# Kernel tuning notes

Hardware: AMD Instinct MI355X
Metric: run time of the kernel (lower is better)

Reference implementation:

```python
import jax, jax.numpy as jnp
import numpy as np
from jax.ops import segment_sum, segment_max

N, E, F, H, G, P, C = 50000, 600000, 128, 128, 64, 32, 10
HEADS = 3
BN_EPS = 1e-5
COS_EPS = 1e-8


def setup_inputs() -> dict:
    key = jax.random.key(0)
    ks = jax.random.split(key, 32)
    rn = lambda k, shape, s: jax.random.normal(k, shape, jnp.float32) * s
    inp = {
        "x": jax.random.normal(ks[0], (N, F), jnp.float32),
        "edge_index": jax.random.randint(ks[1], (2, E), 0, N, jnp.int32),
        "batch": jnp.sort(jax.random.randint(ks[2], (N,), 0, G, jnp.int32)),
        # GCNConv
        "W1": rn(ks[3], (F, H), F ** -0.5), "b1": jnp.zeros((H,), jnp.float32),
        # SAGEConv (lin_l on aggregated neighbors, lin_r on root)
        "Wl": rn(ks[4], (H, H), H ** -0.5), "Wr": rn(ks[5], (H, H), H ** -0.5),
        "bs": jnp.zeros((H,), jnp.float32),
        # GATConv, heads=3, concat=False
        "Wg": rn(ks[6], (H, HEADS * H), H ** -0.5),
        "a_src": rn(ks[7], (HEADS, H), H ** -0.5),
        "a_dst": rn(ks[8], (HEADS, H), H ** -0.5),
        "bg": jnp.zeros((H,), jnp.float32),
        # prototype head / classifier / decoder
        "protos": jax.random.normal(ks[9], (P, H), jnp.float32),
        "Wc": rn(ks[10], (H, C), H ** -0.5), "bc": jnp.zeros((C,), jnp.float32),
        "Wd1": rn(ks[11], (H, 2 * H), H ** -0.5), "bd1": jnp.zeros((2 * H,), jnp.float32),
        "Wd2": rn(ks[12], (2 * H, F), (2 * H) ** -0.5), "bd2": jnp.zeros((F,), jnp.float32),
    }
    # BatchNorm (eval mode): gamma, beta, running mean/var for bn1..bn3
    for i in range(3):
        k0, k1, k2 = jax.random.split(ks[13 + i], 3)
        inp[f"g{i+1}"] = 1.0 + rn(k0, (H,), 0.05)
        inp[f"be{i+1}"] = rn(k1, (H,), 0.05)
        inp[f"m{i+1}"] = rn(k2, (H,), 0.1)
        inp[f"v{i+1}"] = jnp.ones((H,), jnp.float32)
    return inp


def _bn(x, g, b, m, v):
    return (x - m) * jax.lax.rsqrt(v + BN_EPS) * g + b


def _forward(x, edge_index, batch,
             W1, b1, g1, be1, m1, v1,
             Wl, Wr, bs, g2, be2, m2, v2,
             Wg, a_src, a_dst, bg, g3, be3, m3, v3,
             protos, Wc, bc, Wd1, bd1, Wd2, bd2):
    src, dst = edge_index[0], edge_index[1]
    ones_e = jnp.ones((src.shape[0],), x.dtype)

    # --- GCNConv: symmetric norm with self-loops ---
    h = x @ W1                                        # [N, H]
    deg = segment_sum(ones_e, dst, num_segments=N) + 1.0
    dinv = jax.lax.rsqrt(deg)
    coef = dinv[src] * dinv[dst]                      # [E]
    h1 = segment_sum(h[src] * coef[:, None], dst, num_segments=N)
    h1 = h1 + h * (dinv * dinv)[:, None] + b1         # self-loop term + bias
    h1 = jax.nn.elu(_bn(h1, g1, be1, m1, v1))         # dropout = identity (eval)

    # --- SAGEConv: mean aggregation (no self-loops) ---
    cnt = segment_sum(ones_e, dst, num_segments=N)
    mean_nb = segment_sum(h1[src], dst, num_segments=N) / jnp.maximum(cnt, 1.0)[:, None]
    h2 = mean_nb @ Wl + h1 @ Wr + bs
    h2 = jax.nn.elu(_bn(h2, g2, be2, m2, v2))

    # --- GATConv: heads=3, concat=False (mean), with self-loops ---
    hg = (h2 @ Wg).reshape(N, HEADS, H)               # [N, 3, H]
    al_src = jnp.einsum('nhf,hf->nh', hg, a_src)      # [N, 3]
    al_dst = jnp.einsum('nhf,hf->nh', hg, a_dst)
    loop = jnp.arange(N, dtype=src.dtype)
    s2 = jnp.concatenate([src, loop])
    d2 = jnp.concatenate([dst, loop])
    e = jax.nn.leaky_relu(al_src[s2] + al_dst[d2], 0.2)   # [E+N, 3]
    emax = segment_max(e, d2, num_segments=N)             # every node has a self-loop
    ex = jnp.exp(e - emax[d2])
    den = segment_sum(ex, d2, num_segments=N)
    alpha = ex / den[d2]                                  # [E+N, 3]
    h3 = segment_sum(hg[s2] * alpha[:, :, None], d2, num_segments=N)
    h3 = h3.mean(axis=1) + bg                             # concat=False -> head mean
    h3 = jax.nn.elu(_bn(h3, g3, be3, m3, v3))

    # --- global mean pool over graphs ---
    gcnt = segment_sum(jnp.ones((N,), x.dtype), batch, num_segments=G)
    pooled = segment_sum(h3, batch, num_segments=G) / jnp.maximum(gcnt, 1.0)[:, None]

    # --- prototype head: cosine sim -> softmax -> mix ---
    xn = pooled / jnp.maximum(jnp.linalg.norm(pooled, axis=-1, keepdims=True), COS_EPS)
    pn = protos / jnp.maximum(jnp.linalg.norm(protos, axis=-1, keepdims=True), COS_EPS)
    sims = xn @ pn.T                                      # [G, P]
    assignments = jax.nn.softmax(sims, axis=-1)
    proto_emb = assignments @ protos                      # [G, H]
    logits = proto_emb @ Wc + bc                          # [G, C]
    reconstructed = jax.nn.relu(pooled @ Wd1 + bd1) @ Wd2 + bd2   # [G, F]
    return logits, proto_emb, assignments, reconstructed


def reference(x, edge_index, batch,
              W1, b1, g1, be1, m1, v1,
              Wl, Wr, bs, g2, be2, m2, v2,
              Wg, a_src, a_dst, bg, g3, be3, m3, v3,
              protos, Wc, bc, Wd1, bd1, Wd2, bd2):
    return _forward(x, edge_index, batch,
                    W1, b1, g1, be1, m1, v1,
                    Wl, Wr, bs, g2, be2, m2, v2,
                    Wg, a_src, a_dst, bg, g3, be3, m3, v3,
                    protos, Wc, bc, Wd1, bd1, Wd2, bd2)
```

## Files before the change

kernel.cpp:

```cpp
#include <hip/hip_runtime.h>
#include <hip/hip_bf16.h>
#include <stdint.h>
#include <stddef.h>

#define N_ 50000
#define E_ 600000
#define F_ 128
#define H_ 128
#define G_ 64
#define P_ 32
#define C_ 10
#define NB_ 49

typedef __hip_bfloat16 bf16;
typedef __attribute__((ext_vector_type(8))) short short8;
typedef __attribute__((ext_vector_type(4))) float float4v;

__device__ __forceinline__ float b2f(bf16 x){ return __bfloat162float(x); }
__device__ __forceinline__ float us2f(unsigned short u){ return __uint_as_float(((unsigned int)u)<<16); }
__device__ __forceinline__ unsigned short f2us(float x){ bf16 h = __float2bfloat16(x); return *(unsigned short*)&h; }
__device__ __forceinline__ float eluf(float x){ return x>0.f ? x : expm1f(x); }
__device__ __forceinline__ float bnf(float x,float m,float v,float g,float b){ return (x-m)*rsqrtf(v+1e-5f)*g+b; }
__device__ __forceinline__ float lrelu(float x){ return x>0.f ? x : 0.2f*x; }
__device__ __forceinline__ float expc(float x){ return __expf(fminf(x, 50.f)); }
__device__ __forceinline__ void atomAddF(float* a, float v){ unsafeAtomicAdd(a, v); }

__global__ __launch_bounds__(256) void k_wprep(const float* __restrict__ W1, const float* __restrict__ Wl,
    const float* __restrict__ Wr, const float* __restrict__ Wg, unsigned short* __restrict__ WT){
  int idx = blockIdx.x*256 + threadIdx.x;
  if(idx >= 6*16384) return;
  int m = idx >> 14, rem = idx & 16383;
  int n = rem >> 7, k = rem & 127;
  float v;
  if(m==0)      v = W1[k*128+n];
  else if(m==1) v = Wl[k*128+n];
  else if(m==2) v = Wr[k*128+n];
  else          v = Wg[k*384 + (m-3)*128 + n];
  WT[idx] = f2us(v);
}

__device__ __forceinline__ void stage_WT(const unsigned short* __restrict__ WTg, unsigned short* lds, int tid){
  #pragma unroll
  for(int i=0;i<8;i++){
    int idx = tid + i*256;
    int n = idx>>4, c = idx&15;
    uint4 v = *(const uint4*)(WTg + (size_t)idx*8);
    int cs = c ^ (n & 15);
    *(uint4*)(lds + n*128 + cs*8) = v;
  }
}
__device__ __forceinline__ short8 read_Bfrag(const unsigned short* lds, int tile, int kc, int lane){
  int n = tile*16 + (lane&15);
  int c = kc*4 + (lane>>4);
  int cs = c ^ (lane & 15);
  return *(const short8*)(lds + n*128 + cs*8);
}
__device__ __forceinline__ void load_Afrag_bf16(const bf16* A, int row, int lane, short8 af[4]){
  const unsigned short* ap = (const unsigned short*)A + (size_t)row*128 + (lane>>4)*8;
  #pragma unroll
  for(int kc=0;kc<4;kc++) af[kc] = *(const short8*)(ap + kc*32);
}
__device__ __forceinline__ void mfma_pass(const unsigned short* lds, const short8 af[4], int lane, float4v acc[8]){
  #pragma unroll
  for(int tile=0;tile<8;tile++){
    #pragma unroll
    for(int kc=0;kc<4;kc++){
      short8 bfv = read_Bfrag(lds, tile, kc, lane);
      acc[tile] = __builtin_amdgcn_mfma_f32_16x16x32_bf16(af[kc], bfv, acc[tile], 0, 0, 0);
    }
  }
}

__global__ __launch_bounds__(256) void k_mm_x(const float* __restrict__ X, const unsigned short* __restrict__ WTg,
                                              bf16* __restrict__ HB){
  __shared__ unsigned short Wlds[128*128];
  const int tid = threadIdx.x, lane = tid&63, w = tid>>6;
  const int row0 = blockIdx.x*64;
  stage_WT(WTg, Wlds, tid);
  int arow = row0 + w*16 + (lane&15);
  int ar = arow < N_ ? arow : N_-1;
  const float* ap = X + (size_t)ar*128 + (lane>>4)*8;
  short8 af[4];
  #pragma unroll
  for(int kc=0;kc<4;kc++){
    float4 a = *(const float4*)(ap + kc*32);
    float4 b = *(const float4*)(ap + kc*32 + 4);
    short8 v;
    v[0]=(short)f2us(a.x); v[1]=(short)f2us(a.y); v[2]=(short)f2us(a.z); v[3]=(short)f2us(a.w);
    v[4]=(short)f2us(b.x); v[5]=(short)f2us(b.y); v[6]=(short)f2us(b.z); v[7]=(short)f2us(b.w);
    af[kc]=v;
  }
  __syncthreads();
  float4v acc[8];
  #pragma unroll
  for(int t=0;t<8;t++){ acc[t][0]=0.f; acc[t][1]=0.f; acc[t][2]=0.f; acc[t][3]=0.f; }
  mfma_pass(Wlds, af, lane, acc);
  const int colb = lane&15, q = lane>>4;
  unsigned short* ob = (unsigned short*)HB;
  #pragma unroll
  for(int r=0;r<4;r++){
    int ro = row0 + w*16 + q*4 + r;
    if(ro < N_){
      #pragma unroll
      for(int tile=0;tile<8;tile++)
        ob[(size_t)ro*128 + tile*16 + colb] = f2us(acc[tile][r]);
    }
  }
}

__global__ __launch_bounds__(256) void k_sage_mm(const bf16* __restrict__ MaB, const bf16* __restrict__ H1B,
    const unsigned short* __restrict__ WlT, const unsigned short* __restrict__ WrT,
    const float* __restrict__ bs, const float* __restrict__ g2, const float* __restrict__ be2,
    const float* __restrict__ m2, const float* __restrict__ v2, bf16* __restrict__ H2B){
  __shared__ unsigned short Wlds[128*128];
  const int tid = threadIdx.x, lane = tid&63, w = tid>>6;
  const int row0 = blockIdx.x*64;
  int arow = row0 + w*16 + (lane&15);
  int ar = arow < N_ ? arow : N_-1;
  float4v acc[8];
  #pragma unroll
  for(int t=0;t<8;t++){ acc[t][0]=0.f; acc[t][1]=0.f; acc[t][2]=0.f; acc[t][3]=0.f; }
  short8 af[4];

  stage_WT(WlT, Wlds, tid);
  load_Afrag_bf16(MaB, ar, lane, af);
  __syncthreads();
  mfma_pass(Wlds, af, lane, acc);
  __syncthreads();
  stage_WT(WrT, Wlds, tid);
  load_Afrag_bf16(H1B, ar, lane, af);
  __syncthreads();
  mfma_pass(Wlds, af, lane, acc);

  const int colb = lane&15, q = lane>>4;
  unsigned short* ob = (unsigned short*)H2B;
  #pragma unroll
  for(int tile=0;tile<8;tile++){
    int col = tile*16 + colb;
    float bsv=bs[col], gv=g2[col], bev=be2[col], mv=m2[col], vv=v2[col];
    #pragma unroll
    for(int r=0;r<4;r++){
      int ro = row0 + w*16 + q*4 + r;
      if(ro < N_){
        float x = acc[tile][r] + bsv;
        ob[(size_t)ro*128 + col] = f2us(eluf(bnf(x, mv, vv, gv, bev)));
      }
    }
  }
}

__global__ __launch_bounds__(256) void k_gat_mm_all(const bf16* __restrict__ H2B, const unsigned short* __restrict__ WgT,
    const float* __restrict__ a_src, const float* __restrict__ a_dst,
    bf16* __restrict__ HG3, float* __restrict__ als3, float* __restrict__ ald3){
  __shared__ unsigned short Wlds[128*128];
  const int tid = threadIdx.x, lane = tid&63, w = tid>>6;
  const int row0 = blockIdx.x*64;
  int arow = row0 + w*16 + (lane&15);
  int ar = arow < N_ ? arow : N_-1;
  short8 af[4];
  load_Afrag_bf16(H2B, ar, lane, af);
  const int colb = lane&15, q = lane>>4;
  unsigned short* ob = (unsigned short*)HG3;
  for(int hh=0; hh<3; hh++){
    if(hh) __syncthreads();
    stage_WT(WgT + hh*16384, Wlds, tid);
    __syncthreads();
    float4v acc[8];
    #pragma unroll
    for(int t=0;t<8;t++){ acc[t][0]=0.f; acc[t][1]=0.f; acc[t][2]=0.f; acc[t][3]=0.f; }
    mfma_pass(Wlds, af, lane, acc);
    float asv[8], adv[8];
    #pragma unroll
    for(int tile=0;tile<8;tile++){
      asv[tile] = a_src[hh*128 + tile*16 + colb];
      adv[tile] = a_dst[hh*128 + tile*16 + colb];
    }
    #pragma unroll
    for(int r=0;r<4;r++){
      int ro = row0 + w*16 + q*4 + r;
      float ps = 0.f, pd = 0.f;
      #pragma unroll
      for(int tile=0;tile<8;tile++){ ps += acc[tile][r]*asv[tile]; pd += acc[tile][r]*adv[tile]; }
      #pragma unroll
      for(int o=8;o>0;o>>=1){ ps += __shfl_down(ps,o,16); pd += __shfl_down(pd,o,16); }
      if(ro < N_){
        #pragma unroll
        for(int tile=0;tile<8;tile++)
          ob[(size_t)ro*384 + hh*128 + tile*16 + colb] = f2us(acc[tile][r]);
        if(colb == 0){ als3[ro*3+hh] = ps; ald3[ro*3+hh] = pd; }
      }
    }
  }
}

__global__ __launch_bounds__(256) void k_count(const int* __restrict__ dst, int* __restrict__ cnt){
  int e = blockIdx.x*256 + threadIdx.x;
  if(e < E_) atomicAdd(&cnt[dst[e]], 1);
}

__global__ __launch_bounds__(1024) void k_scan1(const int* __restrict__ cnt, int* __restrict__ row_ptr,
                                                float* __restrict__ dinv, int* __restrict__ bsum){
  __shared__ int wsum[16];
  const int t = threadIdx.x, lane = t & 63, wid = t >> 6;
  int i = blockIdx.x*1024 + t;
  int v = (i<N_) ? cnt[i] : 0;
  int x = v;
  #pragma unroll
  for(int o=1;o<64;o<<=1){
    int y = __shfl_up(x, o, 64);
    if(lane >= o) x += y;
  }
  if(lane==63) wsum[wid] = x;
  __syncthreads();
  if(wid==0){
    int s = (lane<16) ? wsum[lane] : 0;
    #pragma unroll
    for(int o=1;o<16;o<<=1){
      int y = __shfl_up(s, o, 64);
      if(lane >= o) s += y;
    }
    if(lane<16) wsum[lane] = s;
  }
  __syncthreads();
  int waveoff = (wid>0) ? wsum[wid-1] : 0;
  int incl = waveoff + x;
  if(i<N_){
    row_ptr[i] = incl - v;
    dinv[i] = rsqrtf((float)v + 1.f);
  }
  if(t==1023) bsum[blockIdx.x] = incl;
}

__global__ __launch_bounds__(64) void k_scan2(const int* __restrict__ bsum, int* __restrict__ boff,
                                              int* __restrict__ row_ptr){
  int lane = threadIdx.x;
  int v = (lane < NB_) ? bsum[lane] : 0;
  int x = v;
  #pragma unroll
  for(int o=1;o<64;o<<=1){
    int y = __shfl_up(x, o, 64);
    if(lane >= o) x += y;
  }
  if(lane < NB_) boff[lane] = x - v;
  if(lane == 63) row_ptr[N_] = x;
}

__global__ __launch_bounds__(256) void k_scan3(int* __restrict__ row_ptr, const int* __restrict__ boff,
                                               int* __restrict__ tmp){
  int i = blockIdx.x*256 + threadIdx.x;
  if(i < N_){
    int r = row_ptr[i] + boff[i>>10];
    row_ptr[i] = r;
    tmp[i] = r;
  }
}

__global__ __launch_bounds__(256) void k_scatter(const int* __restrict__ src, const int* __restrict__ dst,
                                                 int* __restrict__ tmp, int* __restrict__ esrc){
  int e = blockIdx.x*256 + threadIdx.x;
  if(e < E_){
    int d = dst[e];
    int pos = atomicAdd(&tmp[d], 1);
    esrc[pos] = src[e];
  }
}

__global__ __launch_bounds__(256) void k_gcn_gather(const int* __restrict__ row_ptr, const int* __restrict__ esrc,
    const float* __restrict__ dinv, const bf16* __restrict__ HB,
    const float* __restrict__ b1, const float* __restrict__ g1, const float* __restrict__ be1,
    const float* __restrict__ m1, const float* __restrict__ v1, bf16* __restrict__ H1B){
  int n = blockIdx.x*4 + (threadIdx.x>>6);
  int lane = threadIdx.x & 63;
  if(n >= N_) return;
  int beg = row_ptr[n], end = row_ptr[n+1];
  float dn = dinv[n];
  float a0 = 0.f, a1 = 0.f;
  const unsigned short* hb = (const unsigned short*)HB;
  int e = beg;
  for(; e+3 < end; e += 4){
    int s0 = esrc[e], s1 = esrc[e+1], s2 = esrc[e+2], s3 = esrc[e+3];
    unsigned int hv0 = *(const unsigned int*)(hb + (size_t)s0*H_ + lane*2);
    unsigned int hv1 = *(const unsigned int*)(hb + (size_t)s1*H_ + lane*2);
    unsigned int hv2 = *(const unsigned int*)(hb + (size_t)s2*H_ + lane*2);
    unsigned int hv3 = *(const unsigned int*)(hb + (size_t)s3*H_ + lane*2);
    float c0 = dinv[s0]*dn, c1 = dinv[s1]*dn, c2 = dinv[s2]*dn, c3 = dinv[s3]*dn;
    a0 += c0*us2f((unsigned short)(hv0 & 0xFFFFu)) + c1*us2f((unsigned short)(hv1 & 0xFFFFu))
        + c2*us2f((unsigned short)(hv2 & 0xFFFFu)) + c3*us2f((unsigned short)(hv3 & 0xFFFFu));
    a1 += c0*us2f((unsigned short)(hv0 >> 16)) + c1*us2f((unsigned short)(hv1 >> 16))
        + c2*us2f((unsigned short)(hv2 >> 16)) + c3*us2f((unsigned short)(hv3 >> 16));
  }
  for(; e < end; e++){
    int s = esrc[e];
    float c = dinv[s]*dn;
    unsigned int hv = *(const unsigned int*)(hb + (size_t)s*H_ + lane*2);
    a0 += c*us2f((unsigned short)(hv & 0xFFFFu));
    a1 += c*us2f((unsigned short)(hv >> 16));
  }
  unsigned int hv = *(const unsigned int*)(hb + (size_t)n*H_ + lane*2);
  int f0 = lane*2, f1 = f0+1;
  float x0 = a0 + us2f((unsigned short)(hv & 0xFFFFu))*dn*dn + b1[f0];
  float x1 = a1 + us2f((unsigned short)(hv >> 16))*dn*dn + b1[f1];
  x0 = eluf(bnf(x0, m1[f0], v1[f0], g1[f0], be1[f0]));
  x1 = eluf(bnf(x1, m1[f1], v1[f1], g1[f1], be1[f1]));
  unsigned int o = ((unsigned int)f2us(x1)<<16) | f2us(x0);
  *(unsigned int*)((unsigned short*)H1B + (size_t)n*H_ + lane*2) = o;
}

__global__ __launch_bounds__(256) void k_sage_gather(const int* __restrict__ row_ptr, const int* __restrict__ esrc,
    const bf16* __restrict__ H1B, bf16* __restrict__ MeanB){
  int n = blockIdx.x*4 + (threadIdx.x>>6);
  int lane = threadIdx.x & 63;
  if(n >= N_) return;
  int beg = row_ptr[n], end = row_ptr[n+1];
  float a0 = 0.f, a1 = 0.f;
  const unsigned short* hb = (const unsigned short*)H1B;
  int e = beg;
  for(; e+3 < end; e += 4){
    int s0 = esrc[e], s1 = esrc[e+1], s2 = esrc[e+2], s3 = esrc[e+3];
    unsigned int hv0 = *(const unsigned int*)(hb + (size_t)s0*H_ + lane*2);
    unsigned int hv1 = *(const unsigned int*)(hb + (size_t)s1*H_ + lane*2);
    unsigned int hv2 = *(const unsigned int*)(hb + (size_t)s2*H_ + lane*2);
    unsigned int hv3 = *(const unsigned int*)(hb + (size_t)s3*H_ + lane*2);
    a0 += us2f((unsigned short)(hv0 & 0xFFFFu)) + us2f((unsigned short)(hv1 & 0xFFFFu))
        + us2f((unsigned short)(hv2 & 0xFFFFu)) + us2f((unsigned short)(hv3 & 0xFFFFu));
    a1 += us2f((unsigned short)(hv0 >> 16)) + us2f((unsigned short)(hv1 >> 16))
        + us2f((unsigned short)(hv2 >> 16)) + us2f((unsigned short)(hv3 >> 16));
  }
  for(; e < end; e++){
    unsigned int hv = *(const unsigned int*)(hb + (size_t)esrc[e]*H_ + lane*2);
    a0 += us2f((unsigned short)(hv & 0xFFFFu));
    a1 += us2f((unsigned short)(hv >> 16));
  }
  float inv = 1.f / fmaxf((float)(end-beg), 1.f);
  unsigned int o = ((unsigned int)f2us(a1*inv)<<16) | f2us(a0*inv);
  *(unsigned int*)((unsigned short*)MeanB + (size_t)n*H_ + lane*2) = o;
}

__global__ __launch_bounds__(256) void k_gat_gather3(const int* __restrict__ row_ptr, const int* __restrict__ esrc,
    const float* __restrict__ als3, const float* __restrict__ ald3, const bf16* __restrict__ HG3,
    bf16* __restrict__ H3B){
  int n = blockIdx.x*4 + (threadIdx.x>>6);
  int lane = threadIdx.x & 63;
  if(n >= N_) return;
  int beg = row_ptr[n], end = row_ptr[n+1];
  float ald0 = ald3[n*3+0], ald1 = ald3[n*3+1], ald2 = ald3[n*3+2];
  float es0 = expc(lrelu(als3[n*3+0] + ald0));
  float es1 = expc(lrelu(als3[n*3+1] + ald1));
  float es2 = expc(lrelu(als3[n*3+2] + ald2));
  const unsigned short* hb = (const unsigned short*)HG3;
  size_t nb = (size_t)n*384 + lane*2;
  unsigned int h0 = *(const unsigned int*)(hb + nb);
  unsigned int h1 = *(const unsigned int*)(hb + nb + 128);
  unsigned int h2 = *(const unsigned int*)(hb + nb + 256);
  float den0 = es0, den1 = es1, den2 = es2;
  float a00 = es0*us2f((unsigned short)(h0 & 0xFFFFu)), a01 = es0*us2f((unsigned short)(h0 >> 16));
  float a10 = es1*us2f((unsigned short)(h1 & 0xFFFFu)), a11 = es1*us2f((unsigned short)(h1 >> 16));
  float a20 = es2*us2f((unsigned short)(h2 & 0xFFFFu)), a21 = es2*us2f((unsigned short)(h2 >> 16));
  int e = beg;
  for(; e+1 < end; e += 2){
    int s0 = esrc[e], s1 = esrc[e+1];
    size_t b0 = (size_t)s0*384 + lane*2, b1 = (size_t)s1*384 + lane*2;
    unsigned int p00 = *(const unsigned int*)(hb + b0);
    unsigned int p01 = *(const unsigned int*)(hb + b0 + 128);
    unsigned int p02 = *(const unsigned int*)(hb + b0 + 256);
    unsigned int p10 = *(const unsigned int*)(hb + b1);
    unsigned int p11 = *(const unsigned int*)(hb + b1 + 128);
    unsigned int p12 = *(const unsigned int*)(hb + b1 + 256);
    float w00 = expc(lrelu(als3[s0*3+0] + ald0));
    float w01 = expc(lrelu(als3[s0*3+1] + ald1));
    float w02 = expc(lrelu(als3[s0*3+2] + ald2));
    float w10 = expc(lrelu(als3[s1*3+0] + ald0));
    float w11 = expc(lrelu(als3[s1*3+1] + ald1));
    float w12 = expc(lrelu(als3[s1*3+2] + ald2));
    den0 += w00 + w10; den1 += w01 + w11; den2 += w02 + w12;
    a00 += w00*us2f((unsigned short)(p00 & 0xFFFFu)) + w10*us2f((unsigned short)(p10 & 0xFFFFu));
    a01 += w00*us2f((unsigned short)(p00 >> 16))     + w10*us2f((unsigned short)(p10 >> 16));
    a10 += w01*us2f((unsigned short)(p01 & 0xFFFFu)) + w11*us2f((unsigned short)(p11 & 0xFFFFu));
    a11 += w01*us2f((unsigned short)(p01 >> 16))     + w11*us2f((unsigned short)(p11 >> 16));
    a20 += w02*us2f((unsigned short)(p02 & 0xFFFFu)) + w12*us2f((unsigned short)(p12 & 0xFFFFu));
    a21 += w02*us2f((unsigned short)(p02 >> 16))     + w12*us2f((unsigned short)(p12 >> 16));
  }
  if(e < end){
    int s = esrc[e];
    size_t b0 = (size_t)s*384 + lane*2;
    unsigned int p0 = *(const unsigned int*)(hb + b0);
    unsigned int p1 = *(const unsigned int*)(hb + b0 + 128);
    unsigned int p2 = *(const unsigned int*)(hb + b0 + 256);
    float w0 = expc(lrelu(als3[s*3+0] + ald0));
    float w1 = expc(lrelu(als3[s*3+1] + ald1));
    float w2 = expc(lrelu(als3[s*3+2] + ald2));
    den0 += w0; den1 += w1; den2 += w2;
    a00 += w0*us2f((unsigned short)(p0 & 0xFFFFu)); a01 += w0*us2f((unsigned short)(p0 >> 16));
    a10 += w1*us2f((unsigned short)(p1 & 0xFFFFu)); a11 += w1*us2f((unsigned short)(p1 >> 16));
    a20 += w2*us2f((unsigned short)(p2 & 0xFFFFu)); a21 += w2*us2f((unsigned short)(p2 >> 16));
  }
  float i0 = 1.f/(3.f*den0), i1 = 1.f/(3.f*den1), i2 = 1.f/(3.f*den2);
  float r0 = a00*i0 + a10*i1 + a20*i2;
  float r1 = a01*i0 + a11*i1 + a21*i2;
  unsigned int o = ((unsigned int)f2us(r1)<<16) | f2us(r0);
  *(unsigned int*)((unsigned short*)H3B + (size_t)n*H_ + lane*2) = o;
}

#define NPW_ 16
__global__ __launch_bounds__(256) void k_h3fin_pool(const bf16* __restrict__ ACCB, const float* __restrict__ bg,
    const float* __restrict__ g3, const float* __restrict__ be3, const float* __restrict__ m3, const float* __restrict__ v3,
    const int* __restrict__ batch, float* __restrict__ pooled, float* __restrict__ gcnt){
  int wave = blockIdx.x*4 + (threadIdx.x>>6);
  int lane = threadIdx.x & 63;
  int n0 = wave*NPW_;
  if(n0 >= N_) return;
  int n1 = n0 + NPW_; if(n1 > N_) n1 = N_;
  int f0 = lane*2, f1 = f0+1;
  float bg0=bg[f0], bg1=bg[f1];
  float g30=g3[f0], g31=g3[f1], be30=be3[f0], be31=be3[f1];
  float m30=m3[f0], m31=m3[f1], v30=v3[f0], v31=v3[f1];
  float r0=0.f, r1=0.f;
  int cur = batch[n0];
  int seg = 0;
  for(int n=n0; n<n1; n++){
    int b = batch[n];
    if(b != cur){
      atomAddF(&pooled[cur*H_ + f0], r0);
      atomAddF(&pooled[cur*H_ + f1], r1);
      if(lane==0) atomAddF(&gcnt[cur], (float)seg);
      r0 = 0.f; r1 = 0.f; seg = 0; cur = b;
    }
    unsigned int hv = *(const unsigned int*)((const unsigned short*)ACCB + (size_t)n*H_ + lane*2);
    float x0 = us2f((unsigned short)(hv & 0xFFFFu)) + bg0;
    float x1 = us2f((unsigned short)(hv >> 16)) + bg1;
    r0 += eluf(bnf(x0, m30, v30, g30, be30));
    r1 += eluf(bnf(x1, m31, v31, g31, be31));
    seg++;
  }
  atomAddF(&pooled[cur*H_ + f0], r0);
  atomAddF(&pooled[cur*H_ + f1], r1);
  if(lane==0) atomAddF(&gcnt[cur], (float)seg);
}

__global__ __launch_bounds__(128) void k_head(const float* __restrict__ pooledacc, const float* __restrict__ gcnt,
    const float* __restrict__ protos, const float* __restrict__ Wc, const float* __restrict__ bc,
    const float* __restrict__ Wd1, const float* __restrict__ bd1, const float* __restrict__ Wd2, const float* __restrict__ bd2,
    float* __restrict__ out){
  const int g = blockIdx.x, t = threadIdx.x;
  __shared__ float p[128], xn[128], red[128], sims[32], es[32], asg[32], pe[128], t1[256];
  __shared__ float nrm;
  float cg_ = fmaxf(gcnt[g], 1.f);
  p[t] = pooledacc[g*128 + t] / cg_;
  __syncthreads();
  red[t] = p[t]*p[t];
  __syncthreads();
  for(int s=64;s>0;s>>=1){ if(t<s) red[t]+=red[t+s]; __syncthreads(); }
  if(t==0) nrm = fmaxf(sqrtf(red[0]), 1e-8f);
  __syncthreads();
  xn[t] = p[t]/nrm;
  __syncthreads();
  if(t<32){
    float s=0.f, pn=0.f;
    for(int f=0;f<128;f++){ float pv=protos[t*128+f]; s += xn[f]*pv; pn += pv*pv; }
    sims[t] = s / fmaxf(sqrtf(pn), 1e-8f);
  }
  __syncthreads();
  if(t<32){
    float mx=-1e30f;
    for(int j=0;j<32;j++) mx = fmaxf(mx, sims[j]);
    es[t] = __expf(sims[t]-mx);
  }
  __syncthreads();
  if(t<32){
    float sm=0.f;
    for(int j=0;j<32;j++) sm += es[j];
    float a = es[t]/fmaxf(sm,1e-20f);
    asg[t] = a;
    out[8832 + g*32 + t] = a;
  }
  __syncthreads();
  {
    float s=0.f;
    for(int pp=0;pp<32;pp++) s += asg[pp]*protos[pp*128+t];
    pe[t] = s;
    out[640 + g*128 + t] = s;
  }
  __syncthreads();
  if(t<10){
    float s = bc[t];
    for(int f=0;f<128;f++) s += pe[f]*Wc[f*10+t];
    out[g*10 + t] = s;
  }
  for(int j=t;j<256;j+=128){
    float s = bd1[j];
    for(int f=0;f<128;f++) s += p[f]*Wd1[f*256+j];
    t1[j] = fmaxf(s, 0.f);
  }
  __syncthreads();
  {
    float s = bd2[t];
    for(int j=0;j<256;j++) s += t1[j]*Wd2[j*128+t];
    out[10880 + g*128 + t] = s;
  }
}

__global__ void k_sentinel(float* out, float code){
  out[0] = code;
}

extern "C" void kernel_launch(void* const* d_in, const int* in_sizes, int n_in,
                              void* d_out, int out_size, void* d_ws, size_t ws_size,
                              hipStream_t stream){
  const float* X    = (const float*)d_in[0];
  const int*  EI    = (const int*)d_in[1];
  const int*  batch = (const int*)d_in[2];
  const int* src = EI;
  const int* dst = EI + E_;

  int iW1,ib1,iWl,iWr,ibs,iWg,ias,iad,ibg,ipr,iWc,ibc,iWd1,ibd1,iWd2,ibd2;
  int ig1,ibe1,im1,iv1,ig2,ibe2,im2,iv2,ig3,ibe3,im3,iv3;
  if(n_in >= 31 && in_sizes[5] == 128){
    iW1=3; ib1=4; ig1=5; ibe1=6; im1=7; iv1=8;
    iWl=9; iWr=10; ibs=11; ig2=12; ibe2=13; im2=14; iv2=15;
    iWg=16; ias=17; iad=18; ibg=19; ig3=20; ibe3=21; im3=22; iv3=23;
    ipr=24; iWc=25; ibc=26; iWd1=27; ibd1=28; iWd2=29; ibd2=30;
  }else{
    iW1=3; ib1=4; iWl=5; iWr=6; ibs=7; iWg=8; ias=9; iad=10; ibg=11;
    ipr=12; iWc=13; ibc=14; iWd1=15; ibd1=16; iWd2=17; ibd2=18;
    ig1=19; ibe1=20; im1=21; iv1=22; ig2=23; ibe2=24; im2=25; iv2=26;
    ig3=27; ibe3=28; im3=29; iv3=30;
  }
  const float* W1 = (const float*)d_in[iW1];   const float* b1 = (const float*)d_in[ib1];
  const float* Wl = (const float*)d_in[iWl];   const float* Wr = (const float*)d_in[iWr];
  const float* bs = (const float*)d_in[ibs];   const float* Wg = (const float*)d_in[iWg];
  const float* a_src = (const float*)d_in[ias]; const float* a_dst = (const float*)d_in[iad];
  const float* bg = (const float*)d_in[ibg];   const float* protos = (const float*)d_in[ipr];
  const float* Wc = (const float*)d_in[iWc];   const float* bc = (const float*)d_in[ibc];
  const float* Wd1 = (const float*)d_in[iWd1]; const float* bd1 = (const float*)d_in[ibd1];
  const float* Wd2 = (const float*)d_in[iWd2]; const float* bd2 = (const float*)d_in[ibd2];
  const float* g1 = (const float*)d_in[ig1];   const float* be1 = (const float*)d_in[ibe1];
  const float* m1 = (const float*)d_in[im1];   const float* v1 = (const float*)d_in[iv1];
  const float* g2 = (const float*)d_in[ig2];   const float* be2 = (const float*)d_in[ibe2];
  const float* m2 = (const float*)d_in[im2];   const float* v2 = (const float*)d_in[iv2];
  const float* g3 = (const float*)d_in[ig3];   const float* be3 = (const float*)d_in[ibe3];
  const float* m3 = (const float*)d_in[im3];   const float* v3 = (const float*)d_in[iv3];

  const size_t NF = (size_t)N_*H_;
  const size_t intN = (size_t)N_ + (N_+1) + N_ + E_ + 128;
  const size_t fltN = (size_t)6*N_ + G_*H_ + G_;
  const size_t NEED = NF*2*3 + (size_t)N_*384*2 + intN*4 + fltN*4 + (size_t)6*16384*2;
  if(ws_size < NEED){
    k_sentinel<<<1,1,0,stream>>>((float*)d_out, 1000.f + (float)(ws_size>>20));
    return;
  }
  bf16* RA = (bf16*)d_ws;
  bf16* RB = RA + NF;
  bf16* RC = RB + NF;
  bf16* HG3 = RC + NF;
  int*  cnt     = (int*)(HG3 + (size_t)N_*384);
  int*  row_ptr = cnt + N_;
  int*  tmp     = row_ptr + (N_+1);
  int*  esrc    = tmp + N_;
  int*  bsum    = esrc + E_;
  int*  boff    = bsum + 64;
  float* dinv   = (float*)(boff + 64);
  float* als3   = dinv + N_;
  float* ald3   = als3 + (size_t)N_*3;
  float* pooled = ald3 + (size_t)N_*3;
  float* gcnt   = pooled + (size_t)G_*H_;
  unsigned short* WTg = (unsigned short*)(gcnt + G_);

  k_wprep<<<(6*16384+255)/256, 256, 0, stream>>>(W1, Wl, Wr, Wg, WTg);
  hipMemsetAsync(cnt, 0, N_*sizeof(int), stream);
  k_count<<<(E_+255)/256, 256, 0, stream>>>(dst, cnt);
  k_scan1<<<NB_, 1024, 0, stream>>>(cnt, row_ptr, dinv, bsum);
  k_scan2<<<1, 64, 0, stream>>>(bsum, boff, row_ptr);
  k_scan3<<<(N_+255)/256, 256, 0, stream>>>(row_ptr, boff, tmp);
  k_scatter<<<(E_+255)/256, 256, 0, stream>>>(src, dst, tmp, esrc);

  const int GB = (N_+3)/4;
  const int MB = (N_+63)/64;
  k_mm_x<<<MB, 256, 0, stream>>>(X, WTg, RA);
  k_gcn_gather<<<GB, 256, 0, stream>>>(row_ptr, esrc, dinv, RA, b1, g1, be1, m1, v1, RB);
  k_sage_gather<<<GB, 256, 0, stream>>>(row_ptr, esrc, RB, RC);
  k_sage_mm<<<MB, 256, 0, stream>>>(RC, RB, WTg + 16384, WTg + 2*16384, bs, g2, be2, m2, v2, RA);
  k_gat_mm_all<<<MB, 256, 0, stream>>>(RA, WTg + 3*16384, a_src, a_dst, HG3, als3, ald3);
  k_gat_gather3<<<GB, 256, 0, stream>>>(row_ptr, esrc, als3, ald3, HG3, RC);
  hipMemsetAsync(pooled, 0, (size_t)(G_*H_+G_)*sizeof(float), stream);
  {
    int waves = (N_ + NPW_ - 1)/NPW_;
    int blocks = (waves + 3)/4;
    k_h3fin_pool<<<blocks, 256, 0, stream>>>(RC, bg, g3, be3, m3, v3, batch, pooled, gcnt);
  }
  k_head<<<G_, 128, 0, stream>>>(pooled, gcnt, protos, Wc, bc, Wd1, bd1, Wd2, bd2, (float*)d_out);
}
```

Before: 436.5 us.

## Interleave GAT head features and precompute per-edge attention weights in a separate pass

The GAT projection output is stored head-interleaved, so each lane reads its 2 features for all 3 heads with one 12-byte load instead of three scattered 4-byte loads. A new per-edge kernel computes the exp(leaky_relu) attention weights for all heads into a float4 array, using a destination array written during CSR scatter. The gather kernel then streams the precomputed weights and is unrolled by 4. Cheaper bf16 unpack helpers also replace the shift-based conversion. In exchange there is an extra launch plus about 10 MB of edge-weight writes and reads, and extra edst writes during scatter.

```diff
diff --git a/kernel.cpp b/kernel.cpp
--- a/kernel.cpp
+++ b/kernel.cpp
@@ -16,9 +16,13 @@
 typedef __attribute__((ext_vector_type(8))) short short8;
 typedef __attribute__((ext_vector_type(4))) float float4v;
 
+struct __align__(4) u3 { unsigned int x, y, z; };
+
 __device__ __forceinline__ float b2f(bf16 x){ return __bfloat162float(x); }
 __device__ __forceinline__ float us2f(unsigned short u){ return __uint_as_float(((unsigned int)u)<<16); }
 __device__ __forceinline__ unsigned short f2us(float x){ bf16 h = __float2bfloat16(x); return *(unsigned short*)&h; }
+__device__ __forceinline__ float blo(unsigned int u){ return __uint_as_float(u<<16); }
+__device__ __forceinline__ float bhi(unsigned int u){ return __uint_as_float(u & 0xFFFF0000u); }
 __device__ __forceinline__ float eluf(float x){ return x>0.f ? x : expm1f(x); }
 __device__ __forceinline__ float bnf(float x,float m,float v,float g,float b){ return (x-m)*rsqrtf(v+1e-5f)*g+b; }
 __device__ __forceinline__ float lrelu(float x){ return x>0.f ? x : 0.2f*x; }
@@ -151,7 +155,7 @@
 
 __global__ __launch_bounds__(256) void k_gat_mm_all(const bf16* __restrict__ H2B, const unsigned short* __restrict__ WgT,
     const float* __restrict__ a_src, const float* __restrict__ a_dst,
-    bf16* __restrict__ HG3, float* __restrict__ als3, float* __restrict__ ald3){
+    bf16* __restrict__ HG3I, float* __restrict__ als3, float* __restrict__ ald3){
   __shared__ unsigned short Wlds[128*128];
   const int tid = threadIdx.x, lane = tid&63, w = tid>>6;
   const int row0 = blockIdx.x*64;
@@ -160,7 +164,7 @@
   short8 af[4];
   load_Afrag_bf16(H2B, ar, lane, af);
   const int colb = lane&15, q = lane>>4;
-  unsigned short* ob = (unsigned short*)HG3;
+  unsigned short* ob = (unsigned short*)HG3I;
   for(int hh=0; hh<3; hh++){
     if(hh) __syncthreads();
     stage_WT(WgT + hh*16384, Wlds, tid);
@@ -186,7 +190,7 @@
       if(ro < N_){
         #pragma unroll
         for(int tile=0;tile<8;tile++)
-          ob[(size_t)ro*384 + hh*128 + tile*16 + colb] = f2us(acc[tile][r]);
+          ob[(size_t)ro*384 + (size_t)(tile*8 + (colb>>1))*6 + hh*2 + (colb&1)] = f2us(acc[tile][r]);
         if(colb == 0){ als3[ro*3+hh] = ps; ald3[ro*3+hh] = pd; }
       }
     }
@@ -256,13 +260,28 @@
 }
 
 __global__ __launch_bounds__(256) void k_scatter(const int* __restrict__ src, const int* __restrict__ dst,
-                                                 int* __restrict__ tmp, int* __restrict__ esrc){
+                                                 int* __restrict__ tmp, int* __restrict__ esrc,
+                                                 int* __restrict__ edst){
   int e = blockIdx.x*256 + threadIdx.x;
   if(e < E_){
     int d = dst[e];
     int pos = atomicAdd(&tmp[d], 1);
     esrc[pos] = src[e];
-  }
+    edst[pos] = d;
+  }
+}
+
+__global__ __launch_bounds__(256) void k_wexp(const int* __restrict__ esrc, const int* __restrict__ edst,
+    const float* __restrict__ als3, const float* __restrict__ ald3, float* __restrict__ we4){
+  int e = blockIdx.x*256 + threadIdx.x;
+  if(e >= E_) return;
+  int s = esrc[e], d = edst[e];
+  float4 w;
+  w.x = expc(lrelu(als3[s*3+0] + ald3[d*3+0]));
+  w.y = expc(lrelu(als3[s*3+1] + ald3[d*3+1]));
+  w.z = expc(lrelu(als3[s*3+2] + ald3[d*3+2]));
+  w.w = 0.f;
+  *(float4*)(we4 + (size_t)e*4) = w;
 }
 
 __global__ __launch_bounds__(256) void k_gcn_gather(const int* __restrict__ row_ptr, const int* __restrict__ esrc,
@@ -284,22 +303,20 @@
     unsigned int hv2 = *(const unsigned int*)(hb + (size_t)s2*H_ + lane*2);
     unsigned int hv3 = *(const unsigned int*)(hb + (size_t)s3*H_ + lane*2);
     float c0 = dinv[s0]*dn, c1 = dinv[s1]*dn, c2 = dinv[s2]*dn, c3 = dinv[s3]*dn;
-    a0 += c0*us2f((unsigned short)(hv0 & 0xFFFFu)) + c1*us2f((unsigned short)(hv1 & 0xFFFFu))
-        + c2*us2f((unsigned short)(hv2 & 0xFFFFu)) + c3*us2f((unsigned short)(hv3 & 0xFFFFu));
-    a1 += c0*us2f((unsigned short)(hv0 >> 16)) + c1*us2f((unsigned short)(hv1 >> 16))
-        + c2*us2f((unsigned short)(hv2 >> 16)) + c3*us2f((unsigned short)(hv3 >> 16));
+    a0 += c0*blo(hv0) + c1*blo(hv1) + c2*blo(hv2) + c3*blo(hv3);
+    a1 += c0*bhi(hv0) + c1*bhi(hv1) + c2*bhi(hv2) + c3*bhi(hv3);
   }
   for(; e < end; e++){
     int s = esrc[e];
     float c = dinv[s]*dn;
     unsigned int hv = *(const unsigned int*)(hb + (size_t)s*H_ + lane*2);
-    a0 += c*us2f((unsigned short)(hv & 0xFFFFu));
-    a1 += c*us2f((unsigned short)(hv >> 16));
+    a0 += c*blo(hv);
+    a1 += c*bhi(hv);
   }
   unsigned int hv = *(const unsigned int*)(hb + (size_t)n*H_ + lane*2);
   int f0 = lane*2, f1 = f0+1;
-  float x0 = a0 + us2f((unsigned short)(hv & 0xFFFFu))*dn*dn + b1[f0];
-  float x1 = a1 + us2f((unsigned short)(hv >> 16))*dn*dn + b1[f1];
+  float x0 = a0 + blo(hv)*dn*dn + b1[f0];
+  float x1 = a1 + bhi(hv)*dn*dn + b1[f1];
   x0 = eluf(bnf(x0, m1[f0], v1[f0], g1[f0], be1[f0]));
   x1 = eluf(bnf(x1, m1[f1], v1[f1], g1[f1], be1[f1]));
   unsigned int o = ((unsigned int)f2us(x1)<<16) | f2us(x0);
@@ -321,15 +338,13 @@
     unsigned int hv1 = *(const unsigned int*)(hb + (size_t)s1*H_ + lane*2);
     unsigned int hv2 = *(const unsigned int*)(hb + (size_t)s2*H_ + lane*2);
     unsigned int hv3 = *(const unsigned int*)(hb + (size_t)s3*H_ + lane*2);
-    a0 += us2f((unsigned short)(hv0 & 0xFFFFu)) + us2f((unsigned short)(hv1 & 0xFFFFu))
-        + us2f((unsigned short)(hv2 & 0xFFFFu)) + us2f((unsigned short)(hv3 & 0xFFFFu));
-    a1 += us2f((unsigned short)(hv0 >> 16)) + us2f((unsigned short)(hv1 >> 16))
-        + us2f((unsigned short)(hv2 >> 16)) + us2f((unsigned short)(hv3 >> 16));
+    a0 += blo(hv0) + blo(hv1) + blo(hv2) + blo(hv3);
+    a1 += bhi(hv0) + bhi(hv1) + bhi(hv2) + bhi(hv3);
   }
   for(; e < end; e++){
     unsigned int hv = *(const unsigned int*)(hb + (size_t)esrc[e]*H_ + lane*2);
-    a0 += us2f((unsigned short)(hv & 0xFFFFu));
-    a1 += us2f((unsigned short)(hv >> 16));
+    a0 += blo(hv);
+    a1 += bhi(hv);
   }
   float inv = 1.f / fmaxf((float)(end-beg), 1.f);
   unsigned int o = ((unsigned int)f2us(a1*inv)<<16) | f2us(a0*inv);
@@ -337,62 +352,51 @@
 }
 
 __global__ __launch_bounds__(256) void k_gat_gather3(const int* __restrict__ row_ptr, const int* __restrict__ esrc,
-    const float* __restrict__ als3, const float* __restrict__ ald3, const bf16* __restrict__ HG3,
-    bf16* __restrict__ H3B){
+    const float* __restrict__ als3, const float* __restrict__ ald3, const float* __restrict__ we4,
+    const bf16* __restrict__ HG3I, bf16* __restrict__ H3B){
   int n = blockIdx.x*4 + (threadIdx.x>>6);
   int lane = threadIdx.x & 63;
   if(n >= N_) return;
   int beg = row_ptr[n], end = row_ptr[n+1];
-  float ald0 = ald3[n*3+0], ald1 = ald3[n*3+1], ald2 = ald3[n*3+2];
-  float es0 = expc(lrelu(als3[n*3+0] + ald0));
-  float es1 = expc(lrelu(als3[n*3+1] + ald1));
-  float es2 = expc(lrelu(als3[n*3+2] + ald2));
-  const unsigned short* hb = (const unsigned short*)HG3;
-  size_t nb = (size_t)n*384 + lane*2;
-  unsigned int h0 = *(const unsigned int*)(hb + nb);
-  unsigned int h1 = *(const unsigned int*)(hb + nb + 128);
-  unsigned int h2 = *(const unsigned int*)(hb + nb + 256);
+  float es0 = expc(lrelu(als3[n*3+0] + ald3[n*3+0]));
+  float es1 = expc(lrelu(als3[n*3+1] + ald3[n*3+1]));
+  float es2 = expc(lrelu(als3[n*3+2] + ald3[n*3+2]));
+  const unsigned short* hb = (const unsigned short*)HG3I;
+  const int lp6 = lane*6;
+  u3 hs = *(const u3*)(hb + (size_t)n*384 + lp6);
   float den0 = es0, den1 = es1, den2 = es2;
-  float a00 = es0*us2f((unsigned short)(h0 & 0xFFFFu)), a01 = es0*us2f((unsigned short)(h0 >> 16));
-  float a10 = es1*us2f((unsigned short)(h1 & 0xFFFFu)), a11 = es1*us2f((unsigned short)(h1 >> 16));
-  float a20 = es2*us2f((unsigned short)(h2 & 0xFFFFu)), a21 = es2*us2f((unsigned short)(h2 >> 16));
+  float a00 = es0*blo(hs.x), a01 = es0*bhi(hs.x);
+  float a10 = es1*blo(hs.y), a11 = es1*bhi(hs.y);
+  float a20 = es2*blo(hs.z), a21 = es2*bhi(hs.z);
   int e = beg;
-  for(; e+1 < end; e += 2){
-    int s0 = esrc[e], s1 = esrc[e+1];
-    size_t b0 = (size_t)s0*384 + lane*2, b1 = (size_t)s1*384 + lane*2;
-    unsigned int p00 = *(const unsigned int*)(hb + b0);
-    unsigned int p01 = *(const unsigned int*)(hb + b0 + 128);
-    unsigned int p02 = *(const unsigned int*)(hb + b0 + 256);
-    unsigned int p10 = *(const unsigned int*)(hb + b1);
-    unsigned int p11 = *(const unsigned int*)(hb + b1 + 128);
-    unsigned int p12 = *(const unsigned int*)(hb + b1 + 256);
-    float w00 = expc(lrelu(als3[s0*3+0] + ald0));
-    float w01 = expc(lrelu(als3[s0*3+1] + ald1));
-    float w02 = expc(lrelu(als3[s0*3+2] + ald2));
-    float w10 = expc(lrelu(als3[s1*3+0] + ald0));
-    float w11 = expc(lrelu(als3[s1*3+1] + ald1));
-    float w12 = expc(lrelu(als3[s1*3+2] + ald2));
-    den0 += w00 + w10; den1 += w01 + w11; den2 += w02 + w12;
-    a00 += w00*us2f((unsigned short)(p00 & 0xFFFFu)) + w10*us2f((unsigned short)(p10 & 0xFFFFu));
-    a01 += w00*us2f((unsigned short)(p00 >> 16))     + w10*us2f((unsigned short)(p10 >> 16));
-    a10 += w01*us2f((unsigned short)(p01 & 0xFFFFu)) + w11*us2f((unsigned short)(p11 & 0xFFFFu));
-    a11 += w01*us2f((unsigned short)(p01 >> 16))     + w11*us2f((unsigned short)(p11 >> 16));
-    a20 += w02*us2f((unsigned short)(p02 & 0xFFFFu)) + w12*us2f((unsigned short)(p12 & 0xFFFFu));
-    a21 += w02*us2f((unsigned short)(p02 >> 16))     + w12*us2f((unsigned short)(p12 >> 16));
-  }
-  if(e < end){
+  for(; e+3 < end; e += 4){
+    int s0 = esrc[e], s1 = esrc[e+1], s2 = esrc[e+2], s3 = esrc[e+3];
+    float4 w0 = *(const float4*)(we4 + (size_t)(e  )*4);
+    float4 w1 = *(const float4*)(we4 + (size_t)(e+1)*4);
+    float4 w2 = *(const float4*)(we4 + (size_t)(e+2)*4);
+    float4 w3 = *(const float4*)(we4 + (size_t)(e+3)*4);
+    u3 p0 = *(const u3*)(hb + (size_t)s0*384 + lp6);
+    u3 p1 = *(const u3*)(hb + (size_t)s1*384 + lp6);
+    u3 p2 = *(const u3*)(hb + (size_t)s2*384 + lp6);
+    u3 p3 = *(const u3*)(hb + (size_t)s3*384 + lp6);
+    den0 += w0.x + w1.x + w2.x + w3.x;
+    den1 += w0.y + w1.y + w2.y + w3.y;
+    den2 += w0.z + w1.z + w2.z + w3.z;
+    a00 += w0.x*blo(p0.x) + w1.x*blo(p1.x) + w2.x*blo(p2.x) + w3.x*blo(p3.x);
+    a01 += w0.x*bhi(p0.x) + w1.x*bhi(p1.x) + w2.x*bhi(p2.x) + w3.x*bhi(p3.x);
+    a10 += w0.y*blo(p0.y) + w1.y*blo(p1.y) + w2.y*blo(p2.y) + w3.y*blo(p3.y);
+    a11 += w0.y*bhi(p0.y) + w1.y*bhi(p1.y) + w2.y*bhi(p2.y) + w3.y*bhi(p3.y);
+    a20 += w0.z*blo(p0.z) + w1.z*blo(p1.z) + w2.z*blo(p2.z) + w3.z*blo(p3.z);
+    a21 += w0.z*bhi(p0.z) + w1.z*bhi(p1.z) + w2.z*bhi(p2.z) + w3.z*bhi(p3.z);
+  }
+  for(; e < end; e++){
     int s = esrc[e];
-    size_t b0 = (size_t)s*384 + lane*2;
-    unsigned int p0 = *(const unsigned int*)(hb + b0);
-    unsigned int p1 = *(const unsigned int*)(hb + b0 + 128);
-    unsigned int p2 = *(const unsigned int*)(hb + b0 + 256);
-    float w0 = expc(lrelu(als3[s*3+0] + ald0));
-    float w1 = expc(lrelu(als3[s*3+1] + ald1));
-    float w2 = expc(lrelu(als3[s*3+2] + ald2));
-    den0 += w0; den1 += w1; den2 += w2;
-    a00 += w0*us2f((unsigned short)(p0 & 0xFFFFu)); a01 += w0*us2f((unsigned short)(p0 >> 16));
-    a10 += w1*us2f((unsigned short)(p1 & 0xFFFFu)); a11 += w1*us2f((unsigned short)(p1 >> 16));
-    a20 += w2*us2f((unsigned short)(p2 & 0xFFFFu)); a21 += w2*us2f((unsigned short)(p2 >> 16));
+    float4 w = *(const float4*)(we4 + (size_t)e*4);
+    u3 p = *(const u3*)(hb + (size_t)s*384 + lp6);
+    den0 += w.x; den1 += w.y; den2 += w.z;
+    a00 += w.x*blo(p.x); a01 += w.x*bhi(p.x);
+    a10 += w.y*blo(p.y); a11 += w.y*bhi(p.y);
+    a20 += w.z*blo(p.z); a21 += w.z*bhi(p.z);
   }
   float i0 = 1.f/(3.f*den0), i1 = 1.f/(3.f*den1), i2 = 1.f/(3.f*den2);
   float r0 = a00*i0 + a10*i1 + a20*i2;
@@ -426,8 +430,8 @@
       r0 = 0.f; r1 = 0.f; seg = 0; cur = b;
     }
     unsigned int hv = *(const unsigned int*)((const unsigned short*)ACCB + (size_t)n*H_ + lane*2);
-    float x0 = us2f((unsigned short)(hv & 0xFFFFu)) + bg0;
-    float x1 = us2f((unsigned short)(hv >> 16)) + bg1;
+    float x0 = blo(hv) + bg0;
+    float x1 = bhi(hv) + bg1;
     r0 += eluf(bnf(x0, m30, v30, g30, be30));
     r1 += eluf(bnf(x1, m31, v31, g31, be31));
     seg++;
@@ -541,8 +545,8 @@
   const float* m3 = (const float*)d_in[im3];   const float* v3 = (const float*)d_in[iv3];
 
   const size_t NF = (size_t)N_*H_;
-  const size_t intN = (size_t)N_ + (N_+1) + N_ + E_ + 128;
-  const size_t fltN = (size_t)6*N_ + G_*H_ + G_;
+  const size_t intN = (size_t)3*N_ + 4 + (size_t)2*E_ + 128;
+  const size_t fltN = (size_t)7*N_ + (size_t)4*E_ + G_*H_ + G_;
   const size_t NEED = NF*2*3 + (size_t)N_*384*2 + intN*4 + fltN*4 + (size_t)6*16384*2;
   if(ws_size < NEED){
     k_sentinel<<<1,1,0,stream>>>((float*)d_out, 1000.f + (float)(ws_size>>20));
@@ -554,14 +558,16 @@
   bf16* HG3 = RC + NF;
   int*  cnt     = (int*)(HG3 + (size_t)N_*384);
   int*  row_ptr = cnt + N_;
-  int*  tmp     = row_ptr + (N_+1);
+  int*  tmp     = row_ptr + (N_+4);
   int*  esrc    = tmp + N_;
-  int*  bsum    = esrc + E_;
+  int*  edst    = esrc + E_;
+  int*  bsum    = edst + E_;
   int*  boff    = bsum + 64;
   float* dinv   = (float*)(boff + 64);
   float* als3   = dinv + N_;
   float* ald3   = als3 + (size_t)N_*3;
-  float* pooled = ald3 + (size_t)N_*3;
+  float* we4    = ald3 + (size_t)N_*3;
+  float* pooled = we4 + (size_t)E_*4;
   float* gcnt   = pooled + (size_t)G_*H_;
   unsigned short* WTg = (unsigned short*)(gcnt + G_);
 
@@ -571,7 +577,7 @@
   k_scan1<<<NB_, 1024, 0, stream>>>(cnt, row_ptr, dinv, bsum);
   k_scan2<<<1, 64, 0, stream>>>(bsum, boff, row_ptr);
   k_scan3<<<(N_+255)/256, 256, 0, stream>>>(row_ptr, boff, tmp);
-  k_scatter<<<(E_+255)/256, 256, 0, stream>>>(src, dst, tmp, esrc);
+  k_scatter<<<(E_+255)/256, 256, 0, stream>>>(src, dst, tmp, esrc, edst);
 
   const int GB = (N_+3)/4;
   const int MB = (N_+63)/64;
@@ -580,7 +586,8 @@
   k_sage_gather<<<GB, 256, 0, stream>>>(row_ptr, esrc, RB, RC);
   k_sage_mm<<<MB, 256, 0, stream>>>(RC, RB, WTg + 16384, WTg + 2*16384, bs, g2, be2, m2, v2, RA);
   k_gat_mm_all<<<MB, 256, 0, stream>>>(RA, WTg + 3*16384, a_src, a_dst, HG3, als3, ald3);
-  k_gat_gather3<<<GB, 256, 0, stream>>>(row_ptr, esrc, als3, ald3, HG3, RC);
+  k_wexp<<<(E_+255)/256, 256, 0, stream>>>(esrc, edst, als3, ald3, we4);
+  k_gat_gather3<<<GB, 256, 0, stream>>>(row_ptr, esrc, als3, ald3, we4, HG3, RC);
   hipMemsetAsync(pooled, 0, (size_t)(G_*H_+G_)*sizeof(float), stream);
   {
     int waves = (N_ + NPW_ - 1)/NPW_;
```

Measured after the change: 452.4 us. +3.6%, slower.
